# Performance work log

Measured on AMD Instinct MI355X. Metric: run time of the kernel, lower is better.

The kernel has to match this reference:

```python
import jax, jax.numpy as jnp
import numpy as np

N_HEAD = 8
EPS = 1e-5


def setup_inputs() -> dict:
    key = jax.random.key(0)
    ks = jax.random.split(key, 8)
    B, Nq, Ns, C, D = 4, 2048, 2048, 256, 256
    k = jax.random.normal(ks[0], (B, Ns, C), dtype=jnp.float32)
    v = jax.random.normal(ks[1], (B, Ns, D), dtype=jnp.float32)
    q = jax.random.normal(ks[2], (B, Nq, C), dtype=jnp.float32)
    idt = jax.random.normal(ks[3], (B, Nq, D), dtype=jnp.float32)
    s_valid_mask = jax.random.randint(ks[4], (B, Ns), 0, 2, dtype=jnp.int32)
    W_qk = jax.random.normal(ks[5], (C, C), dtype=jnp.float32) / np.sqrt(C)
    W_fc = jax.random.normal(ks[6], (D, D), dtype=jnp.float32) / np.sqrt(D)
    b_fc = jnp.zeros((D,), dtype=jnp.float32)
    ln_w = jnp.ones((D,), dtype=jnp.float32)
    ln_b = jnp.zeros((D,), dtype=jnp.float32)
    return {"k": k, "v": v, "q": q, "idt": idt, "s_valid_mask": s_valid_mask,
            "W_qk": W_qk, "W_fc": W_fc, "b_fc": b_fc, "ln_w": ln_w, "ln_b": ln_b}


def reference(k, v, q, idt, s_valid_mask, W_qk, W_fc, b_fc, ln_w, ln_b):
    B, Nq, C = q.shape
    Ns, D = v.shape[1], v.shape[2]
    H = N_HEAD
    hd = C // H
    temp = hd ** (-0.5)
    # shared qk projection (Linear, no bias): y = x @ W^T
    qh = (q @ W_qk.T).reshape(B, Nq, H, hd)  # bqhd
    kh = (k @ W_qk.T).reshape(B, Ns, H, hd)  # bkhd
    vh = v.reshape(B, Ns, H, D // H)         # bkhd (v_fc is Identity)
    scores = jnp.einsum('bqhd,bkhd->bhqk', qh, kh) * temp
    # additive padding mask: masked (==1) positions get -1000
    mask = s_valid_mask.astype(scores.dtype)[:, None, None, :] * (-1000.0)
    attn = jax.nn.softmax(scores + mask, axis=-1)  # (B,H,Nq,Ns)
    out = jnp.einsum('bhqk,bkhd->bqhd', attn, vh).reshape(B, Nq, D)
    out = out @ W_fc.T + b_fc
    x = out + idt
    mu = jnp.mean(x, axis=-1, keepdims=True)
    var = jnp.mean((x - mu) ** 2, axis=-1, keepdims=True)
    out_ln = (x - mu) * jax.lax.rsqrt(var + EPS) * ln_w + ln_b
    return out_ln, attn.reshape(B * H, Nq, Ns)
```

## Files before the change

### kernel.cpp

```cpp
#include <hip/hip_runtime.h>
#include <hip/hip_bf16.h>

typedef __bf16 bf16;
typedef __attribute__((ext_vector_type(8))) __bf16 b16x8;
typedef __attribute__((ext_vector_type(4))) float f32x4;
typedef __attribute__((ext_vector_type(4))) int i32x4;

#define MFMA16(a, b, c) __builtin_amdgcn_mfma_f32_16x16x32_bf16((a), (b), (c), 0, 0, 0)

#define QSCALE 0.25501568077324936f
#define MCONST -1442.6950408889634f

__global__ void __launch_bounds__(256) k_prep(const float* __restrict__ q,
                                              const float* __restrict__ kk,
                                              const float* __restrict__ Wqk,
                                              const float* __restrict__ v,
                                              const float* __restrict__ Wfc,
                                              const int* __restrict__ svalid,
                                              bf16* __restrict__ ph,
                                              bf16* __restrict__ vT,
                                              bf16* __restrict__ Wfcb,
                                              float* __restrict__ maskf) {
    __shared__ __align__(16) char smem[10240];
    int tid = threadIdx.x;
    int idx = blockIdx.x;
    if (idx < 1024) {
        bf16(*sA)[40] = (bf16(*)[40])smem;
        bf16(*sB)[40] = (bf16(*)[40])(smem + 5120);
        int w = tid >> 6, l = tid & 63, lg = l >> 4, ll = l & 15;
        int wm = w >> 1, wn = w & 1;
        int m0 = (idx & 255) * 64, n0 = (idx >> 8) * 64;
        const float* A = (m0 < 8192) ? q + (size_t)m0 * 256 : kk + (size_t)(m0 - 8192) * 256;
        float osc = (m0 < 8192) ? QSCALE : 1.0f;
        f32x4 acc[2][2] = {};
        int ar = tid >> 2, ac = (tid & 3) * 8;
#pragma unroll
        for (int k0 = 0; k0 < 256; k0 += 32) {
            __syncthreads();
            f32x4 a0 = *(const f32x4*)(A + (size_t)ar * 256 + k0 + ac);
            f32x4 a1 = *(const f32x4*)(A + (size_t)ar * 256 + k0 + ac + 4);
            f32x4 b0 = *(const f32x4*)(Wqk + (size_t)(n0 + ar) * 256 + k0 + ac);
            f32x4 b1 = *(const f32x4*)(Wqk + (size_t)(n0 + ar) * 256 + k0 + ac + 4);
            b16x8 av, bv;
#pragma unroll
            for (int i = 0; i < 4; i++) {
                av[i] = (bf16)a0[i]; av[4 + i] = (bf16)a1[i];
                bv[i] = (bf16)b0[i]; bv[4 + i] = (bf16)b1[i];
            }
            *(b16x8*)&sA[ar][ac] = av;
            *(b16x8*)&sB[ar][ac] = bv;
            __syncthreads();
            b16x8 af[2], bfr[2];
#pragma unroll
            for (int f = 0; f < 2; f++) {
                af[f] = *(b16x8*)&sA[wm * 32 + f * 16 + ll][8 * lg];
                bfr[f] = *(b16x8*)&sB[wn * 32 + f * 16 + ll][8 * lg];
            }
#pragma unroll
            for (int i = 0; i < 2; i++)
#pragma unroll
                for (int j = 0; j < 2; j++) acc[i][j] = MFMA16(af[i], bfr[j], acc[i][j]);
        }
#pragma unroll
        for (int i = 0; i < 2; i++)
#pragma unroll
            for (int j = 0; j < 2; j++) {
                int row = m0 + wm * 32 + i * 16 + lg * 4;
                int col = n0 + wn * 32 + j * 16 + ll;
#pragma unroll
                for (int r = 0; r < 4; r++)
                    ph[(size_t)(row + r) * 256 + col] = (bf16)(acc[i][j][r] * osc);
            }
    } else if (idx < 2048) {
        bf16(*sT)[72] = (bf16(*)[72])smem;
        int i2 = idx - 1024;
        int bh = i2 >> 5, b = bh >> 3, h = bh & 7;
        int ns0 = (i2 & 31) * 64;
        int ns = tid >> 2;
        int dp = (tid & 3) * 8;
        const float* sp = v + ((size_t)(b * 2048 + ns0 + ns)) * 256 + h * 32 + dp;
        f32x4 a = *(const f32x4*)sp;
        f32x4 c = *(const f32x4*)(sp + 4);
#pragma unroll
        for (int i = 0; i < 4; i++) sT[dp + i][ns] = (bf16)a[i];
#pragma unroll
        for (int i = 0; i < 4; i++) sT[dp + 4 + i][ns] = (bf16)c[i];
        __syncthreads();
        int d = tid >> 3;
        int nc = (tid & 7) * 8;
        b16x8 o = *(b16x8*)&sT[d][nc];
        *(b16x8*)(vT + ((size_t)bh * 32 + d) * 2048 + ns0 + nc) = o;
    } else if (idx < 2080) {
        int i = (idx - 2048) * 2048 + tid * 8;
        f32x4 a = *(const f32x4*)(Wfc + i);
        f32x4 b = *(const f32x4*)(Wfc + i + 4);
        b16x8 o;
        o[0] = (bf16)a[0]; o[1] = (bf16)a[1]; o[2] = (bf16)a[2]; o[3] = (bf16)a[3];
        o[4] = (bf16)b[0]; o[5] = (bf16)b[1]; o[6] = (bf16)b[2]; o[7] = (bf16)b[3];
        *(b16x8*)(Wfcb + i) = o;
    } else {
#pragma unroll
        for (int c = 0; c < 32; c++) {
            int i = c * 256 + tid;
            maskf[i] = MCONST * (float)svalid[i];
        }
    }
}

__global__ void __launch_bounds__(256) k_attn(const bf16* __restrict__ ph,
                                              const bf16* __restrict__ vT,
                                              const float* __restrict__ maskf,
                                              bf16* __restrict__ xO,
                                              float* __restrict__ attn) {
    __shared__ __align__(16) bf16 sK[64][40];
    __shared__ __align__(16) bf16 sV[32][72];
    __shared__ __align__(16) float sPf[4][16][68];
    int tid = threadIdx.x;
    int w = tid >> 6, l = tid & 63, lg = l >> 4, ll = l & 15;
    int swz = (blockIdx.x & 7) * 128 + (blockIdx.x >> 3);
    int bh = swz >> 5, qt = swz & 31;
    int b = bh >> 3, h = bh & 7;
    int qrow0 = qt * 64 + w * 16;
    b16x8 qf = *(const b16x8*)(ph + (size_t)(b * 2048 + qrow0 + ll) * 256 + h * 32 + 8 * lg);
    const float* mrow = maskf + b * 2048;
    const bf16* kbase = ph + (size_t)(8192 + b * 2048) * 256 + h * 32;
    const bf16* vbase = vT + (size_t)(bh * 32) * 2048;
    int kr = tid >> 2, kc = (tid & 3) * 8;
    int dr = tid >> 3, nc2 = (tid & 7) * 8;
    float lsum = 0.f;
    {
        *(b16x8*)&sK[kr][kc] = *(const b16x8*)(kbase + (size_t)kr * 256 + kc);
        __syncthreads();
        for (int kt = 0; kt < 2048; kt += 64) {
            bool more = (kt + 64) < 2048;
            b16x8 kst;
            if (more)
                kst = *(const b16x8*)(kbase + (size_t)(kt + 64 + kr) * 256 + kc);
            b16x8 kf[4];
#pragma unroll
            for (int n = 0; n < 4; n++) kf[n] = *(b16x8*)&sK[n * 16 + ll][8 * lg];
            f32x4 s[4];
#pragma unroll
            for (int n = 0; n < 4; n++) {
                f32x4 z = {};
                s[n] = MFMA16(kf[n], qf, z);
            }
#pragma unroll
            for (int n = 0; n < 4; n++) {
                f32x4 mk = *(const f32x4*)&mrow[kt + n * 16 + lg * 4];
#pragma unroll
                for (int r = 0; r < 4; r++) lsum += exp2f(s[n][r] + mk[r]);
            }
            __syncthreads();
            if (more) *(b16x8*)&sK[kr][kc] = kst;
            __syncthreads();
        }
    }
    lsum += __shfl_xor(lsum, 16, 64);
    lsum += __shfl_xor(lsum, 32, 64);
    float linv = 1.f / lsum;
    f32x4 o[2] = {};
    float* outb = attn + (size_t)(bh * 2048 + qrow0) * 2048;
    *(b16x8*)&sK[kr][kc] = *(const b16x8*)(kbase + (size_t)kr * 256 + kc);
    *(b16x8*)&sV[dr][nc2] = *(const b16x8*)(vbase + (size_t)dr * 2048 + nc2);
    __syncthreads();
    for (int kt = 0; kt < 2048; kt += 64) {
        bool more = (kt + 64) < 2048;
        b16x8 kst, vst;
        if (more) {
            kst = *(const b16x8*)(kbase + (size_t)(kt + 64 + kr) * 256 + kc);
            vst = *(const b16x8*)(vbase + (size_t)dr * 2048 + kt + 64 + nc2);
        }
        b16x8 kf[4], vf[2][2];
#pragma unroll
        for (int n = 0; n < 4; n++) kf[n] = *(b16x8*)&sK[n * 16 + ll][8 * lg];
#pragma unroll
        for (int ks = 0; ks < 2; ks++)
#pragma unroll
            for (int j = 0; j < 2; j++)
                vf[ks][j] = *(b16x8*)&sV[j * 16 + ll][ks * 32 + 8 * lg];
        f32x4 s[4];
#pragma unroll
        for (int n = 0; n < 4; n++) {
            f32x4 z = {};
            s[n] = MFMA16(kf[n], qf, z);
        }
#pragma unroll
        for (int n = 0; n < 4; n++) {
            f32x4 mk = *(const f32x4*)&mrow[kt + n * 16 + lg * 4];
            f32x4 ov;
#pragma unroll
            for (int r = 0; r < 4; r++) ov[r] = exp2f(s[n][r] + mk[r]) * linv;
            *(f32x4*)&sPf[w][ll][n * 16 + lg * 4] = ov;
        }
#pragma unroll
        for (int j = 0; j < 4; j++) {
            int row16 = lg + 4 * j;
            f32x4 v = *(f32x4*)&sPf[w][row16][ll * 4];
            __builtin_nontemporal_store(v, (f32x4*)(outb + (size_t)row16 * 2048 + kt + ll * 4));
        }
#pragma unroll
        for (int ks = 0; ks < 2; ks++) {
            f32x4 p0 = *(f32x4*)&sPf[w][ll][ks * 32 + 8 * lg];
            f32x4 p1 = *(f32x4*)&sPf[w][ll][ks * 32 + 8 * lg + 4];
            b16x8 pf;
#pragma unroll
            for (int i = 0; i < 4; i++) {
                pf[i] = (bf16)p0[i];
                pf[4 + i] = (bf16)p1[i];
            }
#pragma unroll
            for (int j = 0; j < 2; j++) o[j] = MFMA16(pf, vf[ks][j], o[j]);
        }
        __syncthreads();
        if (more) {
            *(b16x8*)&sK[kr][kc] = kst;
            *(b16x8*)&sV[dr][nc2] = vst;
        }
        __syncthreads();
    }
#pragma unroll
    for (int r = 0; r < 4; r++) {
        int row = b * 2048 + qrow0 + lg * 4 + r;
#pragma unroll
        for (int j = 0; j < 2; j++) {
            int col = h * 32 + j * 16 + ll;
            xO[(size_t)(row >> 5) * 16384 + (row & 31) * 256 + col] = (bf16)o[j][r];
        }
    }
}

__global__ void __launch_bounds__(256) k_fcln(const bf16* __restrict__ xO,
                                              const bf16* __restrict__ Wfcb,
                                              const float* __restrict__ bias,
                                              const float* __restrict__ idt,
                                              const float* __restrict__ lnw,
                                              const float* __restrict__ lnb,
                                              float* __restrict__ out) {
    __shared__ __align__(16) bf16 sA[32][264];
    __shared__ __align__(16) bf16 sB[256][40];
    __shared__ float sRed[4][32][2];
    int tid = threadIdx.x;
    int w = tid >> 6, l = tid & 63, lg = l >> 4, ll = l & 15;
    int t = blockIdx.x;
#pragma unroll
    for (int c = 0; c < 4; c++) {
        int col = (tid & 7) * 8 + c * 64;
        *(b16x8*)&sA[tid >> 3][col] =
            *(const b16x8*)(xO + (size_t)t * 16384 + (tid >> 3) * 256 + col);
    }
    __syncthreads();
    f32x4 acc[2][4] = {};
#pragma unroll
    for (int k0 = 0; k0 < 256; k0 += 32) {
        if (k0) __syncthreads();
#pragma unroll
        for (int c = 0; c < 4; c++)
            *(b16x8*)&sB[tid][c * 8] = *(const b16x8*)(Wfcb + (size_t)tid * 256 + k0 + c * 8);
        __syncthreads();
        b16x8 af[2];
#pragma unroll
        for (int i = 0; i < 2; i++) af[i] = *(b16x8*)&sA[i * 16 + ll][k0 + 8 * lg];
#pragma unroll
        for (int j = 0; j < 4; j++) {
            b16x8 bfr = *(b16x8*)&sB[w * 64 + j * 16 + ll][8 * lg];
#pragma unroll
            for (int i = 0; i < 2; i++) acc[i][j] = MFMA16(af[i], bfr, acc[i][j]);
        }
    }
    float bcol[4], wcol[4], bbl[4];
#pragma unroll
    for (int j = 0; j < 4; j++) {
        int col = w * 64 + j * 16 + ll;
        bcol[j] = bias[col];
        wcol[j] = lnw[col];
        bbl[j] = lnb[col];
    }
#pragma unroll
    for (int i = 0; i < 2; i++)
#pragma unroll
        for (int r = 0; r < 4; r++) {
            int row32 = i * 16 + lg * 4 + r;
            int grow = t * 32 + row32;
            float a = 0.f, b2 = 0.f;
#pragma unroll
            for (int j = 0; j < 4; j++) {
                float xv = acc[i][j][r] + bcol[j] + idt[(size_t)grow * 256 + w * 64 + j * 16 + ll];
                acc[i][j][r] = xv;
                a += xv;
                b2 += xv * xv;
            }
#pragma unroll
            for (int off = 1; off < 16; off <<= 1) {
                a += __shfl_xor(a, off, 64);
                b2 += __shfl_xor(b2, off, 64);
            }
            if (ll == 0) {
                sRed[w][row32][0] = a;
                sRed[w][row32][1] = b2;
            }
        }
    __syncthreads();
#pragma unroll
    for (int i = 0; i < 2; i++)
#pragma unroll
        for (int r = 0; r < 4; r++) {
            int row32 = i * 16 + lg * 4 + r;
            int grow = t * 32 + row32;
            float st = sRed[0][row32][0] + sRed[1][row32][0] + sRed[2][row32][0] + sRed[3][row32][0];
            float st2 = sRed[0][row32][1] + sRed[1][row32][1] + sRed[2][row32][1] + sRed[3][row32][1];
            float mu = st * (1.f / 256.f);
            float var = st2 * (1.f / 256.f) - mu * mu;
            float rstd = rsqrtf(var + 1e-5f);
#pragma unroll
            for (int j = 0; j < 4; j++)
                out[(size_t)grow * 256 + w * 64 + j * 16 + ll] =
                    (acc[i][j][r] - mu) * rstd * wcol[j] + bbl[j];
        }
}

extern "C" void kernel_launch(void* const* d_in, const int* in_sizes, int n_in,
                              void* d_out, int out_size, void* d_ws, size_t ws_size,
                              hipStream_t stream) {
    const float* k_in = (const float*)d_in[0];
    const float* v_in = (const float*)d_in[1];
    const float* q_in = (const float*)d_in[2];
    const float* idt  = (const float*)d_in[3];
    const int* svalid = (const int*)d_in[4];
    const float* Wqk  = (const float*)d_in[5];
    const float* Wfc  = (const float*)d_in[6];
    const float* bfc  = (const float*)d_in[7];
    const float* lnw  = (const float*)d_in[8];
    const float* lnb  = (const float*)d_in[9];

    float* out_ln = (float*)d_out;
    float* attn = out_ln + 2097152;

    char* ws = (char*)d_ws;
    bf16* ph     = (bf16*)ws;
    bf16* vT     = (bf16*)(ws + 8388608);
    bf16* Wfcb   = (bf16*)(ws + 12582912);
    float* maskf = (float*)(ws + 12713984);

    bf16* xO = (bf16*)out_ln;

    k_prep<<<2081, 256, 0, stream>>>(q_in, k_in, Wqk, v_in, Wfc, svalid, ph, vT, Wfcb, maskf);
    k_attn<<<1024, 256, 0, stream>>>(ph, vT, maskf, xO, attn);
    k_fcln<<<256, 256, 0, stream>>>(xO, Wfcb, bfc, idt, lnw, lnb, out_ln);
}
```

Measured before the change: 173.7 us.

## Double-buffer K/V tiles in attention and halve fc+LN row tile

The attention kernel now double-buffers its shared-memory K and V tiles, so each loop iteration needs one barrier instead of two; the next tile is written into the alternate buffer. The fc+LayerNorm kernel now handles 16 rows per block instead of 32 and launches 512 blocks instead of 256 to fill more compute units. The cost is extra LDS in the attention kernel and the Wfc tiles being reloaded by twice as many blocks in the fc kernel.

```diff
diff --git a/kernel.cpp b/kernel.cpp
--- a/kernel.cpp
+++ b/kernel.cpp
@@ -112,8 +112,8 @@
                                               const float* __restrict__ maskf,
                                               bf16* __restrict__ xO,
                                               float* __restrict__ attn) {
-    __shared__ __align__(16) bf16 sK[64][40];
-    __shared__ __align__(16) bf16 sV[32][72];
+    __shared__ __align__(16) bf16 sK[2][64][40];
+    __shared__ __align__(16) bf16 sV[2][32][72];
     __shared__ __align__(16) float sPf[4][16][68];
     int tid = threadIdx.x;
     int w = tid >> 6, l = tid & 63, lg = l >> 4, ll = l & 15;
@@ -129,8 +129,9 @@
     int dr = tid >> 3, nc2 = (tid & 7) * 8;
     float lsum = 0.f;
     {
-        *(b16x8*)&sK[kr][kc] = *(const b16x8*)(kbase + (size_t)kr * 256 + kc);
+        *(b16x8*)&sK[0][kr][kc] = *(const b16x8*)(kbase + (size_t)kr * 256 + kc);
         __syncthreads();
+        int cur = 0;
         for (int kt = 0; kt < 2048; kt += 64) {
             bool more = (kt + 64) < 2048;
             b16x8 kst;
@@ -138,7 +139,7 @@
                 kst = *(const b16x8*)(kbase + (size_t)(kt + 64 + kr) * 256 + kc);
             b16x8 kf[4];
 #pragma unroll
-            for (int n = 0; n < 4; n++) kf[n] = *(b16x8*)&sK[n * 16 + ll][8 * lg];
+            for (int n = 0; n < 4; n++) kf[n] = *(b16x8*)&sK[cur][n * 16 + ll][8 * lg];
             f32x4 s[4];
 #pragma unroll
             for (int n = 0; n < 4; n++) {
@@ -151,9 +152,9 @@
 #pragma unroll
                 for (int r = 0; r < 4; r++) lsum += exp2f(s[n][r] + mk[r]);
             }
+            if (more) *(b16x8*)&sK[cur ^ 1][kr][kc] = kst;
             __syncthreads();
-            if (more) *(b16x8*)&sK[kr][kc] = kst;
-            __syncthreads();
+            cur ^= 1;
         }
     }
     lsum += __shfl_xor(lsum, 16, 64);
@@ -161,9 +162,10 @@
     float linv = 1.f / lsum;
     f32x4 o[2] = {};
     float* outb = attn + (size_t)(bh * 2048 + qrow0) * 2048;
-    *(b16x8*)&sK[kr][kc] = *(const b16x8*)(kbase + (size_t)kr * 256 + kc);
-    *(b16x8*)&sV[dr][nc2] = *(const b16x8*)(vbase + (size_t)dr * 2048 + nc2);
+    *(b16x8*)&sK[0][kr][kc] = *(const b16x8*)(kbase + (size_t)kr * 256 + kc);
+    *(b16x8*)&sV[0][dr][nc2] = *(const b16x8*)(vbase + (size_t)dr * 2048 + nc2);
     __syncthreads();
+    int cur = 0;
     for (int kt = 0; kt < 2048; kt += 64) {
         bool more = (kt + 64) < 2048;
         b16x8 kst, vst;
@@ -173,12 +175,12 @@
         }
         b16x8 kf[4], vf[2][2];
 #pragma unroll
-        for (int n = 0; n < 4; n++) kf[n] = *(b16x8*)&sK[n * 16 + ll][8 * lg];
+        for (int n = 0; n < 4; n++) kf[n] = *(b16x8*)&sK[cur][n * 16 + ll][8 * lg];
 #pragma unroll
         for (int ks = 0; ks < 2; ks++)
 #pragma unroll
             for (int j = 0; j < 2; j++)
-                vf[ks][j] = *(b16x8*)&sV[j * 16 + ll][ks * 32 + 8 * lg];
+                vf[ks][j] = *(b16x8*)&sV[cur][j * 16 + ll][ks * 32 + 8 * lg];
         f32x4 s[4];
 #pragma unroll
         for (int n = 0; n < 4; n++) {
@@ -212,12 +214,12 @@
 #pragma unroll
             for (int j = 0; j < 2; j++) o[j] = MFMA16(pf, vf[ks][j], o[j]);
         }
+        if (more) {
+            *(b16x8*)&sK[cur ^ 1][kr][kc] = kst;
+            *(b16x8*)&sV[cur ^ 1][dr][nc2] = vst;
+        }
         __syncthreads();
-        if (more) {
-            *(b16x8*)&sK[kr][kc] = kst;
-            *(b16x8*)&sV[dr][nc2] = vst;
-        }
-        __syncthreads();
+        cur ^= 1;
     }
 #pragma unroll
     for (int r = 0; r < 4; r++) {
@@ -237,20 +239,21 @@
                                               const float* __restrict__ lnw,
                                               const float* __restrict__ lnb,
                                               float* __restrict__ out) {
-    __shared__ __align__(16) bf16 sA[32][264];
+    __shared__ __align__(16) bf16 sA[16][264];
     __shared__ __align__(16) bf16 sB[256][40];
-    __shared__ float sRed[4][32][2];
+    __shared__ float sRed[4][16][2];
     int tid = threadIdx.x;
     int w = tid >> 6, l = tid & 63, lg = l >> 4, ll = l & 15;
     int t = blockIdx.x;
-#pragma unroll
-    for (int c = 0; c < 4; c++) {
-        int col = (tid & 7) * 8 + c * 64;
-        *(b16x8*)&sA[tid >> 3][col] =
-            *(const b16x8*)(xO + (size_t)t * 16384 + (tid >> 3) * 256 + col);
+    {
+        const bf16* src = xO + (size_t)(t >> 1) * 16384 + (size_t)((t & 1) * 16) * 256;
+        int r16 = tid >> 4;
+        int c0 = (tid & 15) * 16;
+        *(b16x8*)&sA[r16][c0] = *(const b16x8*)(src + r16 * 256 + c0);
+        *(b16x8*)&sA[r16][c0 + 8] = *(const b16x8*)(src + r16 * 256 + c0 + 8);
     }
     __syncthreads();
-    f32x4 acc[2][4] = {};
+    f32x4 acc[4] = {};
 #pragma unroll
     for (int k0 = 0; k0 < 256; k0 += 32) {
         if (k0) __syncthreads();
@@ -258,14 +261,11 @@
         for (int c = 0; c < 4; c++)
             *(b16x8*)&sB[tid][c * 8] = *(const b16x8*)(Wfcb + (size_t)tid * 256 + k0 + c * 8);
         __syncthreads();
-        b16x8 af[2];
-#pragma unroll
-        for (int i = 0; i < 2; i++) af[i] = *(b16x8*)&sA[i * 16 + ll][k0 + 8 * lg];
+        b16x8 af = *(b16x8*)&sA[ll][k0 + 8 * lg];
 #pragma unroll
         for (int j = 0; j < 4; j++) {
             b16x8 bfr = *(b16x8*)&sB[w * 64 + j * 16 + ll][8 * lg];
-#pragma unroll
-            for (int i = 0; i < 2; i++) acc[i][j] = MFMA16(af[i], bfr, acc[i][j]);
+            acc[j] = MFMA16(af, bfr, acc[j]);
         }
     }
     float bcol[4], wcol[4], bbl[4];
@@ -277,46 +277,42 @@
         bbl[j] = lnb[col];
     }
 #pragma unroll
-    for (int i = 0; i < 2; i++)
-#pragma unroll
-        for (int r = 0; r < 4; r++) {
-            int row32 = i * 16 + lg * 4 + r;
-            int grow = t * 32 + row32;
-            float a = 0.f, b2 = 0.f;
-#pragma unroll
-            for (int j = 0; j < 4; j++) {
-                float xv = acc[i][j][r] + bcol[j] + idt[(size_t)grow * 256 + w * 64 + j * 16 + ll];
-                acc[i][j][r] = xv;
-                a += xv;
-                b2 += xv * xv;
-            }
-#pragma unroll
-            for (int off = 1; off < 16; off <<= 1) {
-                a += __shfl_xor(a, off, 64);
-                b2 += __shfl_xor(b2, off, 64);
-            }
-            if (ll == 0) {
-                sRed[w][row32][0] = a;
-                sRed[w][row32][1] = b2;
-            }
-        }
+    for (int r = 0; r < 4; r++) {
+        int row16 = lg * 4 + r;
+        int grow = t * 16 + row16;
+        float a = 0.f, b2 = 0.f;
+#pragma unroll
+        for (int j = 0; j < 4; j++) {
+            float xv = acc[j][r] + bcol[j] + idt[(size_t)grow * 256 + w * 64 + j * 16 + ll];
+            acc[j][r] = xv;
+            a += xv;
+            b2 += xv * xv;
+        }
+#pragma unroll
+        for (int off = 1; off < 16; off <<= 1) {
+            a += __shfl_xor(a, off, 64);
+            b2 += __shfl_xor(b2, off, 64);
+        }
+        if (ll == 0) {
+            sRed[w][row16][0] = a;
+            sRed[w][row16][1] = b2;
+        }
+    }
     __syncthreads();
 #pragma unroll
-    for (int i = 0; i < 2; i++)
-#pragma unroll
-        for (int r = 0; r < 4; r++) {
-            int row32 = i * 16 + lg * 4 + r;
-            int grow = t * 32 + row32;
-            float st = sRed[0][row32][0] + sRed[1][row32][0] + sRed[2][row32][0] + sRed[3][row32][0];
-            float st2 = sRed[0][row32][1] + sRed[1][row32][1] + sRed[2][row32][1] + sRed[3][row32][1];
-            float mu = st * (1.f / 256.f);
-            float var = st2 * (1.f / 256.f) - mu * mu;
-            float rstd = rsqrtf(var + 1e-5f);
-#pragma unroll
-            for (int j = 0; j < 4; j++)
-                out[(size_t)grow * 256 + w * 64 + j * 16 + ll] =
-                    (acc[i][j][r] - mu) * rstd * wcol[j] + bbl[j];
-        }
+    for (int r = 0; r < 4; r++) {
+        int row16 = lg * 4 + r;
+        int grow = t * 16 + row16;
+        float st = sRed[0][row16][0] + sRed[1][row16][0] + sRed[2][row16][0] + sRed[3][row16][0];
+        float st2 = sRed[0][row16][1] + sRed[1][row16][1] + sRed[2][row16][1] + sRed[3][row16][1];
+        float mu = st * (1.f / 256.f);
+        float var = st2 * (1.f / 256.f) - mu * mu;
+        float rstd = rsqrtf(var + 1e-5f);
+#pragma unroll
+        for (int j = 0; j < 4; j++)
+            out[(size_t)grow * 256 + w * 64 + j * 16 + ll] =
+                (acc[j][r] - mu) * rstd * wcol[j] + bbl[j];
+    }
 }
 
 extern "C" void kernel_launch(void* const* d_in, const int* in_sizes, int n_in,
@@ -346,5 +342,5 @@
 
     k_prep<<<2081, 256, 0, stream>>>(q_in, k_in, Wqk, v_in, Wfc, svalid, ph, vT, Wfcb, maskf);
     k_attn<<<1024, 256, 0, stream>>>(ph, vT, maskf, xO, attn);
-    k_fcln<<<256, 256, 0, stream>>>(xO, Wfcb, bfc, idt, lnw, lnb, out_ln);
+    k_fcln<<<512, 256, 0, stream>>>(xO, Wfcb, bfc, idt, lnw, lnb, out_ln);
 }
```

Result: no change. 175.1 us (+0.8%).
